# Kernel tuning notes

Measured on AMD Instinct MI355X. Metric: run time of the kernel, lower is better.

The kernel has to match this reference:

```python
import jax, jax.numpy as jnp
import numpy as np
import math

B, S, H, NH = 2, 4096, 768, 12
HD = H // NH  # 64
LN_EPS = 1e-12


def setup_inputs() -> dict:
    key = jax.random.key(0)
    ks = jax.random.split(key, 6)
    scale = 0.02
    return {
        "hidden_states": jax.random.normal(ks[0], (B, S, H), jnp.float32),
        "attention_mask": jnp.zeros((B, 1, 1, S), jnp.float32),
        "q_w": jax.random.normal(ks[1], (H, H), jnp.float32) * scale,
        "q_b": jnp.zeros((H,), jnp.float32),
        "k_w": jax.random.normal(ks[2], (H, H), jnp.float32) * scale,
        "k_b": jnp.zeros((H,), jnp.float32),
        "v_w": jax.random.normal(ks[3], (H, H), jnp.float32) * scale,
        "v_b": jnp.zeros((H,), jnp.float32),
        "o_w": jax.random.normal(ks[4], (H, H), jnp.float32) * scale,
        "o_b": jnp.zeros((H,), jnp.float32),
        "ln_g": jnp.ones((H,), jnp.float32),
        "ln_b": jnp.zeros((H,), jnp.float32),
    }


def _heads(x):
    # [B,S,H] -> [B,NH,S,HD]
    return x.reshape(B, S, NH, HD).transpose(0, 2, 1, 3)


def reference(hidden_states, attention_mask, q_w, q_b, k_w, k_b, v_w, v_b,
              o_w, o_b, ln_g, ln_b):
    q = _heads(hidden_states @ q_w.T + q_b)
    k = _heads(hidden_states @ k_w.T + k_b)
    v = _heads(hidden_states @ v_w.T + v_b)

    scores = jnp.einsum("bhqd,bhkd->bhqk", q, k) / math.sqrt(HD)
    scores = scores + attention_mask  # additive mask, broadcast [B,1,1,S]
    probs = jax.nn.softmax(scores, axis=-1)  # dropout p=0 in eval
    ctx = jnp.einsum("bhqk,bhkd->bhqd", probs, v)
    ctx = ctx.transpose(0, 2, 1, 3).reshape(B, S, H)

    # Residual block: dense -> (dropout p=0) -> LN(x + input)
    y = ctx @ o_w.T + o_b + hidden_states
    mu = jnp.mean(y, axis=-1, keepdims=True)
    var = jnp.mean(jnp.square(y - mu), axis=-1, keepdims=True)
    out = (y - mu) * jax.lax.rsqrt(var + LN_EPS) * ln_g + ln_b
    return out
```

## Files before the change

kernel.cpp:

```cpp
#include <hip/hip_runtime.h>

typedef __bf16 bf16;
typedef __bf16 bf16x4 __attribute__((ext_vector_type(4)));
typedef __bf16 bf16x8 __attribute__((ext_vector_type(8)));
typedef float f32x4 __attribute__((ext_vector_type(4)));
typedef float f32x16 __attribute__((ext_vector_type(16)));

#define NB 2
#define SEQ 4096
#define HID 768
#define NHEAD 12
#define HDIM 64
#define MTOT (NB * SEQ)
#define LOG2E 1.4426950408889634f

__device__ inline void pack_body(const float* __restrict__ in, bf16* __restrict__ out, int rt) {
    __shared__ alignas(16) bf16 T[16 * 264];
    const int lane = threadIdx.x;
    const int c = lane & 15, g = lane >> 4;
    const float4* in4 = (const float4*)in + (size_t)rt * 16 * (HID / 4);
    for (int chunk = 0; chunk < 3; chunk++) {
#pragma unroll
        for (int i = 0; i < 16; i++) {
            float4 v = in4[(size_t)i * (HID / 4) + chunk * 64 + lane];
            bf16x4 o;
            o[0] = (bf16)v.x; o[1] = (bf16)v.y; o[2] = (bf16)v.z; o[3] = (bf16)v.w;
            *(bf16x4*)&T[i * 264 + lane * 4] = o;
        }
        __syncthreads();
#pragma unroll
        for (int s = 0; s < 8; s++) {
            bf16x8 val = *(const bf16x8*)&T[c * 264 + s * 32 + g * 8];
            *(bf16x8*)(out + (((size_t)rt * 24 + chunk * 8 + s) * 64 + lane) * 8) = val;
        }
        __syncthreads();
    }
}

__global__ __launch_bounds__(64) void pack_a(const float* __restrict__ in, bf16* __restrict__ out) {
    pack_body(in, out, blockIdx.x);
}

__global__ __launch_bounds__(64) void pack_w4(
    const float* __restrict__ w0, const float* __restrict__ w1,
    const float* __restrict__ w2, const float* __restrict__ w3,
    bf16* __restrict__ o0, bf16* __restrict__ o1, bf16* __restrict__ o2, bf16* __restrict__ o3) {
    int y = blockIdx.y;
    const float* in = (y == 0) ? w0 : (y == 1) ? w1 : (y == 2) ? w2 : w3;
    bf16* out = (y == 0) ? o0 : (y == 1) ? o1 : (y == 2) ? o2 : o3;
    pack_body(in, out, blockIdx.x);
}

__global__ __launch_bounds__(256) void pack_mask(const float* __restrict__ mask,
                                                 float* __restrict__ mp) {
    int idx = blockIdx.x * 256 + threadIdx.x;
    int b = idx >> 12, r = idx & 4095;
    int kt = r >> 5, hi = (r >> 4) & 1, i = r & 15;
    int k = kt * 32 + (i & 3) + 8 * (i >> 2) + 4 * hi;
    mp[idx] = mask[b * SEQ + k] * LOG2E;
}

__global__ __launch_bounds__(256, 2) void qkv_gemm(
    const bf16* __restrict__ Xp,
    const bf16* __restrict__ Wq, const bf16* __restrict__ Wk, const bf16* __restrict__ Wv,
    const float* __restrict__ bq, const float* __restrict__ bk, const float* __restrict__ bv,
    bf16* __restrict__ Qh, bf16* __restrict__ Kh, bf16* __restrict__ Vt)
{
    int z = blockIdx.z;
    const bf16* W = (z == 0) ? Wq : (z == 1) ? Wk : Wv;
    const float* bias = (z == 0) ? bq : (z == 1) ? bk : bv;

    int lane = threadIdx.x & 63;
    int wid  = threadIdx.x >> 6;
    int wm = wid >> 1, wn = wid & 1;
    int g = lane >> 4, c = lane & 15;
    int m0 = blockIdx.y * 128 + wm * 64;
    int n0 = blockIdx.x * 128 + wn * 64;

    f32x4 acc[4][4] = {};
    const bf16* Ap = Xp + ((size_t)(m0 >> 4) * 24) * 512 + (size_t)lane * 8;
    const bf16* Bp = W  + ((size_t)(n0 >> 4) * 24) * 512 + (size_t)lane * 8;

    for (int ks = 0; ks < 24; ks++) {
        bf16x8 a[4], b[4];
#pragma unroll
        for (int i = 0; i < 4; i++) {
            a[i] = *(const bf16x8*)(Ap + ((size_t)i * 24 + ks) * 512);
            b[i] = *(const bf16x8*)(Bp + ((size_t)i * 24 + ks) * 512);
        }
#pragma unroll
        for (int mi = 0; mi < 4; mi++)
#pragma unroll
            for (int ni = 0; ni < 4; ni++)
                acc[mi][ni] = __builtin_amdgcn_mfma_f32_16x16x32_bf16(a[mi], b[ni], acc[mi][ni], 0, 0, 0);
    }

#pragma unroll
    for (int ni = 0; ni < 4; ni++) {
        int n = n0 + ni * 16 + c;
        float bval = bias[n];
        int h = n >> 6, d = n & 63;
#pragma unroll
        for (int mi = 0; mi < 4; mi++) {
#pragma unroll
            for (int j = 0; j < 4; j++) {
                int m = m0 + mi * 16 + g * 4 + j;
                float val = acc[mi][ni][j] + bval;
                int bb = m >> 12, s = m & 4095;
                size_t bhb = (size_t)(bb * NHEAD + h) * SEQ * HDIM;
                if (z == 0) {
                    val *= 0.125f * LOG2E;
                    Qh[bhb + (size_t)s * HDIM + d] = (bf16)val;
                } else if (z == 1) {
                    int fragidx = (((s >> 5) & 1) << 2) | (d >> 4);
                    int lane2 = (s & 31) | (((d >> 3) & 1) << 5);
                    Kh[bhb + (size_t)(s >> 6) * 4096 + fragidx * 512 + lane2 * 8 + (d & 7)] = (bf16)val;
                } else {
                    int fragidx = ((d >> 5) << 2) | ((s >> 4) & 3);
                    int lane2 = (d & 31) | (((s >> 3) & 1) << 5);
                    Vt[bhb + (size_t)(s >> 6) * 4096 + fragidx * 512 + lane2 * 8 + (s & 7)] = (bf16)val;
                }
            }
        }
    }
}

__device__ inline float xhalf_max(float x) {
    float a_ = x, b_ = x;
    asm("v_permlane32_swap_b32 %0, %1" : "+v"(a_), "+v"(b_));
    return fmaxf(a_, b_);
}

__device__ inline void smax16(f32x16& s, float& m, f32x16& o0, f32x16& o1, f32x16& la) {
    float t0 = fmaxf(fmaxf(s[0], s[1]), s[2]);
    float t1 = fmaxf(fmaxf(s[3], s[4]), s[5]);
    float t2 = fmaxf(fmaxf(s[6], s[7]), s[8]);
    float t3 = fmaxf(fmaxf(s[9], s[10]), s[11]);
    float t4 = fmaxf(fmaxf(s[12], s[13]), s[14]);
    float u0 = fmaxf(fmaxf(t0, t1), t2);
    float u1 = fmaxf(fmaxf(t3, t4), s[15]);
    float t = xhalf_max(fmaxf(u0, u1));
    if (__any(t > m + 8.f)) {
        float mn = fmaxf(m, t);
        float al = __builtin_amdgcn_exp2f(m - mn);
        m = mn;
#pragma unroll
        for (int i = 0; i < 16; i++) { o0[i] *= al; o1[i] *= al; la[i] *= al; }
    }
#pragma unroll
    for (int i = 0; i < 16; i++) s[i] = __builtin_amdgcn_exp2f(s[i] - m);
}

__device__ inline void pconv16(const f32x16& sc, bf16x8* pa) {
    unsigned u[8];
#pragma unroll
    for (int i = 0; i < 8; i++) {
        union { bf16 hh[2]; unsigned uu; } x;
        x.hh[0] = (bf16)sc[i * 2];
        x.hh[1] = (bf16)sc[i * 2 + 1];
        u[i] = x.uu;
    }
    asm("v_permlane32_swap_b32 %0, %1" : "+v"(u[0]), "+v"(u[2]));
    asm("v_permlane32_swap_b32 %0, %1" : "+v"(u[1]), "+v"(u[3]));
    asm("v_permlane32_swap_b32 %0, %1" : "+v"(u[4]), "+v"(u[6]));
    asm("v_permlane32_swap_b32 %0, %1" : "+v"(u[5]), "+v"(u[7]));
    union { unsigned uu[4]; bf16x8 v; } f0, f1;
    f0.uu[0] = u[0]; f0.uu[1] = u[1]; f0.uu[2] = u[2]; f0.uu[3] = u[3];
    f1.uu[0] = u[4]; f1.uu[1] = u[5]; f1.uu[2] = u[6]; f1.uu[3] = u[7];
    pa[0] = f0.v;
    pa[1] = f1.v;
}

__global__ __launch_bounds__(256, 4) void attn_kernel(
    const bf16* __restrict__ Qh, const bf16* __restrict__ Kh, const bf16* __restrict__ Vt,
    const float* __restrict__ maskp, bf16* __restrict__ ctxp)
{
    __shared__ float Sm[2][2048];
    __shared__ float Sml[2][128];
    __shared__ alignas(16) bf16 Ep[2][2048];

    const int lane = threadIdx.x & 63;
    const int wid = threadIdx.x >> 6;
    const int qg = wid >> 1;
    const int kp = wid & 1;
    const int lq = lane & 31;
    const int hi = lane >> 5;
    const int bh = blockIdx.x;
    const int b = bh / NHEAD, h = bh % NHEAD;
    const size_t base = (size_t)bh * SEQ * HDIM;
    const int qw = blockIdx.y * 64 + qg * 32;

    bf16x8 qf[4];
#pragma unroll
    for (int dc = 0; dc < 4; dc++)
        qf[dc] = *(const bf16x8*)(Qh + base + (size_t)(qw + lq) * HDIM + dc * 16 + hi * 8);

    const bf16* kfrag = Kh + base + (size_t)lane * 8;
    const bf16* vfrag = Vt + base + (size_t)lane * 8;
    const float* mbase = maskp + ((size_t)b * 128 * 2 + hi) * 16;

    bf16x8 ones;
#pragma unroll
    for (int j = 0; j < 8; j++) ones[j] = (bf16)1.0f;

    float m = -3e38f;
    f32x16 o0 = {}, o1 = {}, la = {};

    for (int t = 0; t < SEQ / 64; t++) {
        const int kt = 2 * t + kp;
        const size_t tb = (size_t)(kt >> 1) * 4096;
        const int khalf = kt & 1;

        bf16x8 kf[4];
#pragma unroll
        for (int dc = 0; dc < 4; dc++)
            kf[dc] = *(const bf16x8*)(kfrag + tb + (khalf * 4 + dc) * 512);

        f32x16 s = *(const f32x16*)(mbase + (size_t)kt * 32);

        __builtin_amdgcn_s_setprio(1);
#pragma unroll
        for (int dc = 0; dc < 4; dc++)
            s = __builtin_amdgcn_mfma_f32_32x32x16_bf16(kf[dc], qf[dc], s, 0, 0, 0);
        __builtin_amdgcn_s_setprio(0);

        bf16x8 vf[4];
        vf[0] = *(const bf16x8*)(vfrag + tb + (khalf * 2 + 0) * 512);
        vf[1] = *(const bf16x8*)(vfrag + tb + (khalf * 2 + 1) * 512);
        vf[2] = *(const bf16x8*)(vfrag + tb + (4 + khalf * 2 + 0) * 512);
        vf[3] = *(const bf16x8*)(vfrag + tb + (4 + khalf * 2 + 1) * 512);

        smax16(s, m, o0, o1, la);
        bf16x8 pa[2];
        pconv16(s, pa);

        __builtin_amdgcn_s_setprio(1);
        la = __builtin_amdgcn_mfma_f32_32x32x16_bf16(ones, pa[0], la, 0, 0, 0);
        la = __builtin_amdgcn_mfma_f32_32x32x16_bf16(ones, pa[1], la, 0, 0, 0);
        o0 = __builtin_amdgcn_mfma_f32_32x32x16_bf16(vf[0], pa[0], o0, 0, 0, 0);
        o0 = __builtin_amdgcn_mfma_f32_32x32x16_bf16(vf[1], pa[1], o0, 0, 0, 0);
        o1 = __builtin_amdgcn_mfma_f32_32x32x16_bf16(vf[2], pa[0], o1, 0, 0, 0);
        o1 = __builtin_amdgcn_mfma_f32_32x32x16_bf16(vf[3], pa[1], o1, 0, 0, 0);
        __builtin_amdgcn_s_setprio(0);
    }

    float l = la[0];

    if (kp == 1) {
#pragma unroll
        for (int i = 0; i < 16; i++) {
            Sm[qg][i * 64 + lane]        = o0[i];
            Sm[qg][(16 + i) * 64 + lane] = o1[i];
        }
        Sml[qg][lane] = m; Sml[qg][64 + lane] = l;
    }
    __syncthreads();
    if (kp == 1) return;

    {
        float mB = Sml[qg][lane], lB = Sml[qg][64 + lane];
        float mm = fmaxf(m, mB);
        float a = __builtin_amdgcn_exp2f(m - mm);
        float bb_ = __builtin_amdgcn_exp2f(mB - mm);
        l = l * a + lB * bb_;
#pragma unroll
        for (int i = 0; i < 16; i++) {
            o0[i] = o0[i] * a + Sm[qg][i * 64 + lane] * bb_;
            o1[i] = o1[i] * a + Sm[qg][(16 + i) * 64 + lane] * bb_;
        }
    }

    float inv = 1.f / l;
    bf16* ep = Ep[qg];
    const int sw = (lq & 7) << 4;
#pragma unroll
    for (int g = 0; g < 4; g++) {
        bf16x4 p0, p1;
#pragma unroll
        for (int j = 0; j < 4; j++) {
            p0[j] = (bf16)(o0[g * 4 + j] * inv);
            p1[j] = (bf16)(o1[g * 4 + j] * inv);
        }
        int colb = g * 16 + hi * 8;
        *(bf16x4*)((char*)ep + lq * 128 + (colb ^ sw)) = p0;
        *(bf16x4*)((char*)ep + lq * 128 + ((64 + colb) ^ sw)) = p1;
    }
    const int c = lane & 15, gg = lane >> 4;
#pragma unroll
    for (int mt = 0; mt < 2; mt++) {
#pragma unroll
        for (int s2 = 0; s2 < 2; s2++) {
            int row = mt * 16 + c;
            int colb = (s2 * 64 + gg * 16) ^ ((row & 7) << 4);
            bf16x8 val = *(const bf16x8*)((const char*)ep + row * 128 + colb);
            size_t mtg = (size_t)((b * SEQ + qw) >> 4) + mt;
            *(bf16x8*)(ctxp + ((mtg * 24 + h * 2 + s2) * 64 + lane) * 8) = val;
        }
    }
}

__global__ __launch_bounds__(256, 2) void oproj_gemm(
    const bf16* __restrict__ Cp, const bf16* __restrict__ Wo, const float* __restrict__ bo,
    const float* __restrict__ hidden, float* __restrict__ y)
{
    int lane = threadIdx.x & 63;
    int wid  = threadIdx.x >> 6;
    int wm = wid >> 1, wn = wid & 1;
    int g = lane >> 4, c = lane & 15;
    int m0 = blockIdx.y * 128 + wm * 64;
    int n0 = blockIdx.x * 128 + wn * 64;

    f32x4 acc[4][4] = {};
    const bf16* Ap = Cp + ((size_t)(m0 >> 4) * 24) * 512 + (size_t)lane * 8;
    const bf16* Bp = Wo + ((size_t)(n0 >> 4) * 24) * 512 + (size_t)lane * 8;

    for (int ks = 0; ks < 24; ks++) {
        bf16x8 a[4], b[4];
#pragma unroll
        for (int i = 0; i < 4; i++) {
            a[i] = *(const bf16x8*)(Ap + ((size_t)i * 24 + ks) * 512);
            b[i] = *(const bf16x8*)(Bp + ((size_t)i * 24 + ks) * 512);
        }
#pragma unroll
        for (int mi = 0; mi < 4; mi++)
#pragma unroll
            for (int ni = 0; ni < 4; ni++)
                acc[mi][ni] = __builtin_amdgcn_mfma_f32_16x16x32_bf16(a[mi], b[ni], acc[mi][ni], 0, 0, 0);
    }

#pragma unroll
    for (int ni = 0; ni < 4; ni++) {
        int n = n0 + ni * 16 + c;
        float bval = bo[n];
#pragma unroll
        for (int mi = 0; mi < 4; mi++) {
#pragma unroll
            for (int j = 0; j < 4; j++) {
                int m = m0 + mi * 16 + g * 4 + j;
                size_t idx = (size_t)m * HID + n;
                y[idx] = acc[mi][ni][j] + bval + hidden[idx];
            }
        }
    }
}

__global__ __launch_bounds__(256) void ln_kernel(
    const float* __restrict__ y, const float* __restrict__ gam,
    const float* __restrict__ bet, float* __restrict__ out)
{
    int row = blockIdx.x * 4 + (threadIdx.x >> 6);
    int lane = threadIdx.x & 63;
    const float* yr = y + (size_t)row * HID;

    float4 v[3];
#pragma unroll
    for (int i = 0; i < 3; i++)
        v[i] = reinterpret_cast<const float4*>(yr)[lane + i * 64];

    float s = 0.f;
#pragma unroll
    for (int i = 0; i < 3; i++) s += v[i].x + v[i].y + v[i].z + v[i].w;
#pragma unroll
    for (int msk = 1; msk < 64; msk <<= 1) s += __shfl_xor(s, msk, 64);
    float mean = s * (1.f / 768.f);

    float q = 0.f;
#pragma unroll
    for (int i = 0; i < 3; i++) {
        float dx = v[i].x - mean, dy = v[i].y - mean, dz = v[i].z - mean, dw = v[i].w - mean;
        q += dx * dx + dy * dy + dz * dz + dw * dw;
    }
#pragma unroll
    for (int msk = 1; msk < 64; msk <<= 1) q += __shfl_xor(q, msk, 64);
    float rstd = rsqrtf(q * (1.f / 768.f) + 1e-12f);

    float* outr = out + (size_t)row * HID;
#pragma unroll
    for (int i = 0; i < 3; i++) {
        float4 gg = reinterpret_cast<const float4*>(gam)[lane + i * 64];
        float4 bb = reinterpret_cast<const float4*>(bet)[lane + i * 64];
        float4 o;
        o.x = (v[i].x - mean) * rstd * gg.x + bb.x;
        o.y = (v[i].y - mean) * rstd * gg.y + bb.y;
        o.z = (v[i].z - mean) * rstd * gg.z + bb.z;
        o.w = (v[i].w - mean) * rstd * gg.w + bb.w;
        reinterpret_cast<float4*>(outr)[lane + i * 64] = o;
    }
}

extern "C" void kernel_launch(void* const* d_in, const int* in_sizes, int n_in,
                              void* d_out, int out_size, void* d_ws, size_t ws_size,
                              hipStream_t stream) {
    const float* hidden = (const float*)d_in[0];
    const float* mask   = (const float*)d_in[1];
    const float* q_w = (const float*)d_in[2];
    const float* q_b = (const float*)d_in[3];
    const float* k_w = (const float*)d_in[4];
    const float* k_b = (const float*)d_in[5];
    const float* v_w = (const float*)d_in[6];
    const float* v_b = (const float*)d_in[7];
    const float* o_w = (const float*)d_in[8];
    const float* o_b = (const float*)d_in[9];
    const float* ln_g = (const float*)d_in[10];
    const float* ln_b = (const float*)d_in[11];
    float* out = (float*)d_out;

    const size_t SZ_X = (size_t)MTOT * HID;
    const size_t SZ_W = (size_t)HID * HID;

    char* ws = (char*)d_ws;
    size_t XB_OFF = 0;
    size_t W_OFF  = XB_OFF + SZ_X * 2;
    size_t QH_OFF = W_OFF + 4 * SZ_W * 2;
    size_t KH_OFF = QH_OFF + SZ_X * 2;
    size_t VT_OFF = KH_OFF + SZ_X * 2;
    size_t MP_OFF = VT_OFF + SZ_X * 2;

    bf16* Xp  = (bf16*)(ws + XB_OFF);
    bf16* Wqp = (bf16*)(ws + W_OFF);
    bf16* Wkp = Wqp + SZ_W;
    bf16* Wvp = Wkp + SZ_W;
    bf16* Wop = Wvp + SZ_W;
    bf16* Qh  = (bf16*)(ws + QH_OFF);
    bf16* Kh  = (bf16*)(ws + KH_OFF);
    bf16* Vt  = (bf16*)(ws + VT_OFF);
    float* Mp = (float*)(ws + MP_OFF);
    bf16* ctxp = (bf16*)(ws + XB_OFF);
    float* y  = (float*)(ws + QH_OFF);

    pack_a<<<dim3(MTOT / 16), 64, 0, stream>>>(hidden, Xp);
    pack_w4<<<dim3(HID / 16, 4), 64, 0, stream>>>(q_w, k_w, v_w, o_w, Wqp, Wkp, Wvp, Wop);
    pack_mask<<<dim3(32), 256, 0, stream>>>(mask, Mp);

    qkv_gemm<<<dim3(HID / 128, MTOT / 128, 3), 256, 0, stream>>>(
        Xp, Wqp, Wkp, Wvp, q_b, k_b, v_b, Qh, Kh, Vt);

    attn_kernel<<<dim3(NB * NHEAD, SEQ / 64), 256, 0, stream>>>(Qh, Kh, Vt, Mp, ctxp);

    oproj_gemm<<<dim3(HID / 128, MTOT / 128), 256, 0, stream>>>(ctxp, Wop, o_b, hidden, y);

    ln_kernel<<<dim3(MTOT / 4), 256, 0, stream>>>(y, ln_g, ln_b, out);
}
```

Measured before the change: 290.7 us.

## Fold additive mask into V scaling and row-sum weights; double-buffer K fragments

The additive mask is turned into multiplicative weights exp(mask), which are applied to V during the QKV GEMM epilogue and used as the A-operand of the row-sum MFMA in place of a ones vector. This drops the per-tile f32x16 mask load that seeded the score accumulator. The attention loop is also unrolled by two with K fragments prefetched one tile ahead, and the occupancy hint drops from 4 to 3 blocks. Because the row max now ignores the mask and the weights are rounded to bf16, large negative or varied masks may behave differently numerically.

```diff
diff --git a/kernel.cpp b/kernel.cpp
--- a/kernel.cpp
+++ b/kernel.cpp
@@ -51,19 +51,20 @@
     pack_body(in, out, blockIdx.x);
 }
 
-__global__ __launch_bounds__(256) void pack_mask(const float* __restrict__ mask,
-                                                 float* __restrict__ mp) {
+__global__ __launch_bounds__(256) void prep_mask(const float* __restrict__ mask,
+                                                 float* __restrict__ wexp,
+                                                 bf16* __restrict__ wp) {
     int idx = blockIdx.x * 256 + threadIdx.x;
-    int b = idx >> 12, r = idx & 4095;
-    int kt = r >> 5, hi = (r >> 4) & 1, i = r & 15;
-    int k = kt * 32 + (i & 3) + 8 * (i >> 2) + 4 * hi;
-    mp[idx] = mask[b * SEQ + k] * LOG2E;
+    float w = exp2f(mask[idx] * LOG2E);
+    wexp[idx] = w;
+    wp[idx] = (bf16)w;
 }
 
 __global__ __launch_bounds__(256, 2) void qkv_gemm(
     const bf16* __restrict__ Xp,
     const bf16* __restrict__ Wq, const bf16* __restrict__ Wk, const bf16* __restrict__ Wv,
     const float* __restrict__ bq, const float* __restrict__ bk, const float* __restrict__ bv,
+    const float* __restrict__ wexp,
     bf16* __restrict__ Qh, bf16* __restrict__ Kh, bf16* __restrict__ Vt)
 {
     int z = blockIdx.z;
@@ -116,6 +117,7 @@
                     int lane2 = (s & 31) | (((d >> 3) & 1) << 5);
                     Kh[bhb + (size_t)(s >> 6) * 4096 + fragidx * 512 + lane2 * 8 + (d & 7)] = (bf16)val;
                 } else {
+                    val *= wexp[bb * SEQ + s];
                     int fragidx = ((d >> 5) << 2) | ((s >> 4) & 3);
                     int lane2 = (d & 31) | (((s >> 3) & 1) << 5);
                     Vt[bhb + (size_t)(s >> 6) * 4096 + fragidx * 512 + lane2 * 8 + (s & 7)] = (bf16)val;
@@ -171,9 +173,9 @@
     pa[1] = f1.v;
 }
 
-__global__ __launch_bounds__(256, 4) void attn_kernel(
+__global__ __launch_bounds__(256, 3) void attn_kernel(
     const bf16* __restrict__ Qh, const bf16* __restrict__ Kh, const bf16* __restrict__ Vt,
-    const float* __restrict__ maskp, bf16* __restrict__ ctxp)
+    const bf16* __restrict__ wp, bf16* __restrict__ ctxp)
 {
     __shared__ float Sm[2][2048];
     __shared__ float Sml[2][128];
@@ -197,52 +199,60 @@
 
     const bf16* kfrag = Kh + base + (size_t)lane * 8;
     const bf16* vfrag = Vt + base + (size_t)lane * 8;
-    const float* mbase = maskp + ((size_t)b * 128 * 2 + hi) * 16;
-
-    bf16x8 ones;
-#pragma unroll
-    for (int j = 0; j < 8; j++) ones[j] = (bf16)1.0f;
+    const bf16* wrow = wp + b * SEQ + hi * 8;
 
     float m = -3e38f;
     f32x16 o0 = {}, o1 = {}, la = {};
 
-    for (int t = 0; t < SEQ / 64; t++) {
-        const int kt = 2 * t + kp;
-        const size_t tb = (size_t)(kt >> 1) * 4096;
-        const int khalf = kt & 1;
-
-        bf16x8 kf[4];
+    bf16x8 kfA[4], kfB[4];
+    {
+        const size_t tb0 = (size_t)(kp >> 1) * 4096;
+        const int kh0 = kp & 1;
 #pragma unroll
         for (int dc = 0; dc < 4; dc++)
-            kf[dc] = *(const bf16x8*)(kfrag + tb + (khalf * 4 + dc) * 512);
-
-        f32x16 s = *(const f32x16*)(mbase + (size_t)kt * 32);
-
-        __builtin_amdgcn_s_setprio(1);
-#pragma unroll
-        for (int dc = 0; dc < 4; dc++)
-            s = __builtin_amdgcn_mfma_f32_32x32x16_bf16(kf[dc], qf[dc], s, 0, 0, 0);
-        __builtin_amdgcn_s_setprio(0);
-
-        bf16x8 vf[4];
-        vf[0] = *(const bf16x8*)(vfrag + tb + (khalf * 2 + 0) * 512);
-        vf[1] = *(const bf16x8*)(vfrag + tb + (khalf * 2 + 1) * 512);
-        vf[2] = *(const bf16x8*)(vfrag + tb + (4 + khalf * 2 + 0) * 512);
-        vf[3] = *(const bf16x8*)(vfrag + tb + (4 + khalf * 2 + 1) * 512);
-
-        smax16(s, m, o0, o1, la);
-        bf16x8 pa[2];
-        pconv16(s, pa);
-
-        __builtin_amdgcn_s_setprio(1);
-        la = __builtin_amdgcn_mfma_f32_32x32x16_bf16(ones, pa[0], la, 0, 0, 0);
-        la = __builtin_amdgcn_mfma_f32_32x32x16_bf16(ones, pa[1], la, 0, 0, 0);
-        o0 = __builtin_amdgcn_mfma_f32_32x32x16_bf16(vf[0], pa[0], o0, 0, 0, 0);
-        o0 = __builtin_amdgcn_mfma_f32_32x32x16_bf16(vf[1], pa[1], o0, 0, 0, 0);
-        o1 = __builtin_amdgcn_mfma_f32_32x32x16_bf16(vf[2], pa[0], o1, 0, 0, 0);
-        o1 = __builtin_amdgcn_mfma_f32_32x32x16_bf16(vf[3], pa[1], o1, 0, 0, 0);
-        __builtin_amdgcn_s_setprio(0);
-    }
+            kfA[dc] = *(const bf16x8*)(kfrag + tb0 + (kh0 * 4 + dc) * 512);
+    }
+
+#define ITER(T, KFC, KFN)                                                                 \
+    {                                                                                     \
+        const int kt = 2 * (T) + kp;                                                      \
+        const size_t tb = (size_t)(kt >> 1) * 4096;                                       \
+        const int khalf = kt & 1;                                                         \
+        f32x16 s = {};                                                                    \
+        _Pragma("unroll")                                                                 \
+        for (int dc = 0; dc < 4; dc++)                                                    \
+            s = __builtin_amdgcn_mfma_f32_32x32x16_bf16(KFC[dc], qf[dc], s, 0, 0, 0);     \
+        {                 \
+            const int kn = kt + 2;                                                        \
+            const size_t tbn = (size_t)(kn >> 1) * 4096;                                  \
+            const int khn = kn & 1;                                                       \
+            _Pragma("unroll")                                                             \
+            for (int dc = 0; dc < 4; dc++)                                                \
+                KFN[dc] = *(const bf16x8*)(kfrag + tbn + (khn * 4 + dc) * 512);           \
+        }                                                                                 \
+        bf16x8 vf[4];                                                                     \
+        vf[0] = *(const bf16x8*)(vfrag + tb + (khalf * 2 + 0) * 512);                     \
+        vf[1] = *(const bf16x8*)(vfrag + tb + (khalf * 2 + 1) * 512);                     \
+        vf[2] = *(const bf16x8*)(vfrag + tb + (4 + khalf * 2 + 0) * 512);                 \
+        vf[3] = *(const bf16x8*)(vfrag + tb + (4 + khalf * 2 + 1) * 512);                 \
+        bf16x8 wf0 = *(const bf16x8*)(wrow + kt * 32);                                    \
+        bf16x8 wf1 = *(const bf16x8*)(wrow + kt * 32 + 16);                               \
+        smax16(s, m, o0, o1, la);                                                         \
+        bf16x8 pa[2];                                                                     \
+        pconv16(s, pa);                                                                   \
+        la = __builtin_amdgcn_mfma_f32_32x32x16_bf16(wf0, pa[0], la, 0, 0, 0);            \
+        la = __builtin_amdgcn_mfma_f32_32x32x16_bf16(wf1, pa[1], la, 0, 0, 0);            \
+        o0 = __builtin_amdgcn_mfma_f32_32x32x16_bf16(vf[0], pa[0], o0, 0, 0, 0);          \
+        o0 = __builtin_amdgcn_mfma_f32_32x32x16_bf16(vf[1], pa[1], o0, 0, 0, 0);          \
+        o1 = __builtin_amdgcn_mfma_f32_32x32x16_bf16(vf[2], pa[0], o1, 0, 0, 0);          \
+        o1 = __builtin_amdgcn_mfma_f32_32x32x16_bf16(vf[3], pa[1], o1, 0, 0, 0);          \
+    }
+
+    for (int t = 0; t < SEQ / 64; t += 2) {
+        ITER(t, kfA, kfB);
+        ITER(t + 1, kfB, kfA);
+    }
+#undef ITER
 
     float l = la[0];
 
@@ -414,7 +424,8 @@
     size_t QH_OFF = W_OFF + 4 * SZ_W * 2;
     size_t KH_OFF = QH_OFF + SZ_X * 2;
     size_t VT_OFF = KH_OFF + SZ_X * 2;
-    size_t MP_OFF = VT_OFF + SZ_X * 2;
+    size_t WE_OFF = VT_OFF + SZ_X * 2;
+    size_t WP_OFF = WE_OFF + (size_t)MTOT * 4;
 
     bf16* Xp  = (bf16*)(ws + XB_OFF);
     bf16* Wqp = (bf16*)(ws + W_OFF);
@@ -424,18 +435,19 @@
     bf16* Qh  = (bf16*)(ws + QH_OFF);
     bf16* Kh  = (bf16*)(ws + KH_OFF);
     bf16* Vt  = (bf16*)(ws + VT_OFF);
-    float* Mp = (float*)(ws + MP_OFF);
+    float* wexp = (float*)(ws + WE_OFF);
+    bf16* wp  = (bf16*)(ws + WP_OFF);
     bf16* ctxp = (bf16*)(ws + XB_OFF);
     float* y  = (float*)(ws + QH_OFF);
 
     pack_a<<<dim3(MTOT / 16), 64, 0, stream>>>(hidden, Xp);
     pack_w4<<<dim3(HID / 16, 4), 64, 0, stream>>>(q_w, k_w, v_w, o_w, Wqp, Wkp, Wvp, Wop);
-    pack_mask<<<dim3(32), 256, 0, stream>>>(mask, Mp);
+    prep_mask<<<dim3(MTOT / 256), 256, 0, stream>>>(mask, wexp, wp);
 
     qkv_gemm<<<dim3(HID / 128, MTOT / 128, 3), 256, 0, stream>>>(
-        Xp, Wqp, Wkp, Wvp, q_b, k_b, v_b, Qh, Kh, Vt);
-
-    attn_kernel<<<dim3(NB * NHEAD, SEQ / 64), 256, 0, stream>>>(Qh, Kh, Vt, Mp, ctxp);
+        Xp, Wqp, Wkp, Wvp, q_b, k_b, v_b, wexp, Qh, Kh, Vt);
+
+    attn_kernel<<<dim3(NB * NHEAD, SEQ / 64), 256, 0, stream>>>(Qh, Kh, Vt, wp, ctxp);
 
     oproj_gemm<<<dim3(HID / 128, MTOT / 128), 256, 0, stream>>>(ctxp, Wop, o_b, hidden, y);
 
```

Result: faster. 273.6 us (-5.9%).
